# Optimization experiments

Measured on AMD Instinct MI355X. Metric: run time of the kernel, lower is better.

## Reference

```python
import jax, jax.numpy as jnp
import numpy as np
from jax import lax


def _lstm_cell(x, h, c, Wih, Whh, bih, bhh):
    # PyTorch LSTM gate order: i, f, g, o
    g = x @ Wih.T + h @ Whh.T + bih + bhh
    i, f, gg, o = jnp.split(g, 4, axis=-1)
    c_new = jax.nn.sigmoid(f) * c + jax.nn.sigmoid(i) * jnp.tanh(gg)
    h_new = jax.nn.sigmoid(o) * jnp.tanh(c_new)
    return h_new, c_new


def setup_inputs() -> dict:
    key = jax.random.key(0)
    B, Tm1, I, H, D = 2048, 32, 512, 1024, 1024
    E = H
    ks = jax.random.split(key, 20)
    s = 0.05
    return {
        'X': jax.random.normal(ks[0], (B, Tm1, I), jnp.float32),
        'y_prev': jax.random.normal(ks[1], (B, Tm1), jnp.float32),
        'enc_attn_w': jax.random.normal(ks[2], (1, 2 * H + Tm1), jnp.float32) * s,
        'enc_attn_b': jax.random.normal(ks[3], (1,), jnp.float32) * s,
        'Wih_e': jax.random.normal(ks[4], (4 * H, I), jnp.float32) * s,
        'Whh_e': jax.random.normal(ks[5], (4 * H, H), jnp.float32) * s,
        'bih_e': jax.random.normal(ks[6], (4 * H,), jnp.float32) * s,
        'bhh_e': jax.random.normal(ks[7], (4 * H,), jnp.float32) * s,
        'W1': jax.random.normal(ks[8], (E, 2 * D + E), jnp.float32) * s,
        'b1': jax.random.normal(ks[9], (E,), jnp.float32) * s,
        'W2': jax.random.normal(ks[10], (1, E), jnp.float32) * s,
        'b2': jax.random.normal(ks[11], (1,), jnp.float32) * s,
        'Wih_d': jax.random.normal(ks[12], (4 * D, 1), jnp.float32) * s,
        'Whh_d': jax.random.normal(ks[13], (4 * D, D), jnp.float32) * s,
        'bih_d': jax.random.normal(ks[14], (4 * D,), jnp.float32) * s,
        'bhh_d': jax.random.normal(ks[15], (4 * D,), jnp.float32) * s,
        'fc_w': jax.random.normal(ks[16], (1, E + 1), jnp.float32) * s,
        'fc_b': jax.random.normal(ks[17], (1,), jnp.float32) * s,
        'ff_w': jax.random.normal(ks[18], (1, D + E), jnp.float32) * s,
        'ff_b': jax.random.normal(ks[19], (1,), jnp.float32) * s,
    }


def reference(X, y_prev, enc_attn_w, enc_attn_b, Wih_e, Whh_e, bih_e, bhh_e,
              W1, b1, W2, b2, Wih_d, Whh_d, bih_d, bhh_d, fc_w, fc_b, ff_w, ff_b):
    B, Tm1, I = X.shape
    H = Whh_e.shape[1]
    D = Whh_d.shape[1]
    E = H
    dt = X.dtype

    # ---------------- Encoder ----------------
    # encoder_attn weight acts on [h; s; X_perm_row]; split for efficiency
    w_h = enc_attn_w[0, :H]
    w_s = enc_attn_w[0, H:2 * H]
    w_x = enc_attn_w[0, 2 * H:]
    # X part of attention logits is step-independent: [B, I]
    xw = jnp.einsum('bti,t->bi', X, w_x)

    def enc_step(carry, x_t):  # x_t: [B, I]
        h, s = carry
        base = h @ w_h + s @ w_s + enc_attn_b[0]          # [B]
        alpha = jax.nn.softmax(base[:, None] + xw, -1)    # softmax over input_size
        x_tilde = alpha * x_t                             # [B, I]
        h_new, s_new = _lstm_cell(x_tilde, h, s, Wih_e, Whh_e, bih_e, bhh_e)
        return (h_new, s_new), (x_tilde, h_new)

    z = jnp.zeros((B, H), dt)
    (_, _), (X_tilde, X_enc) = lax.scan(enc_step, (z, z), jnp.swapaxes(X, 0, 1))
    X_enc = jnp.swapaxes(X_enc, 0, 1)   # [B, T-1, E]

    # ---------------- Decoder ----------------
    W1_dc = W1[:, :2 * D]   # acts on [d; c]
    W1_x = W1[:, 2 * D:]    # acts on X_encoded
    Xenc_proj = jnp.einsum('bte,fe->btf', X_enc, W1_x) + b1  # [B, T-1, E]
    w2 = W2[0]

    def dec_step(carry, y_t):  # y_t: [B]
        d, c = carry
        pre = jnp.concatenate([d, c], -1) @ W1_dc.T          # [B, E]
        scores = jnp.tanh(pre[:, None, :] + Xenc_proj) @ w2 + b2[0]  # [B, T-1]
        beta = jax.nn.softmax(scores, -1)
        context = jnp.einsum('bt,bte->be', beta, X_enc)      # [B, E]
        y_tilde = context @ fc_w[0, :E] + y_t * fc_w[0, E] + fc_b[0]  # [B]
        d_new, c_new = _lstm_cell(y_tilde[:, None], d, c, Wih_d, Whh_d, bih_d, bhh_d)
        return (d_new, c_new), context

    zd = jnp.zeros((B, D), dt)
    (d, _), contexts = lax.scan(dec_step, (zd, zd), y_prev.T)
    context = contexts[-1]                                   # [B, E]
    y_pred = jnp.concatenate([d, context], -1) @ ff_w[0] + ff_b[0]  # [B]
    return y_pred[:, None]
```

## Files before the change

### kernel.cpp

```cpp
#include <hip/hip_runtime.h>
#include <cstddef>
#include <cstdint>


#define B_ 2048
#define T_ 32
#define I_ 512
#define H_ 1024
#define G_ 4096
#define E_ 1024

typedef unsigned short u16;
typedef float f32x4 __attribute__((ext_vector_type(4)));
typedef short bf16x8 __attribute__((ext_vector_type(8)));
typedef __attribute__((address_space(1))) const void gv_t;
typedef __attribute__((address_space(3))) void lv_t;

__device__ __forceinline__ float bf2f(u16 u) {
    union { float f; unsigned v; } w; w.v = ((unsigned)u) << 16; return w.f;
}
__device__ __forceinline__ u16 f2bf(float f) {
    union { float f; unsigned v; } w; w.f = f;
    unsigned r = w.v + 0x7fff + ((w.v >> 16) & 1);
    return (u16)(r >> 16);
}
template <typename T>
__device__ __forceinline__ float ld1(const T* p) {
    if constexpr (sizeof(T) == 4) return *(const float*)p;
    else return bf2f(*(const u16*)p);
}
template <typename T>
__device__ __forceinline__ float4 ld4(const T* p) {
    if constexpr (sizeof(T) == 4) {
        return *(const float4*)p;
    } else {
        const ushort4 u = *(const ushort4*)p;
        float4 r; r.x = bf2f(u.x); r.y = bf2f(u.y); r.z = bf2f(u.z); r.w = bf2f(u.w);
        return r;
    }
}
__device__ __forceinline__ float tf(float x) {
    const float e = __expf(2.0f * x);
    return 1.0f - 2.0f / (e + 1.0f);
}
__device__ __forceinline__ float sg(float x) {
    return 1.0f / (1.0f + __expf(-x));
}

__device__ __forceinline__ int lds_off(int row, int k) {
    return row * 128 + ((k * 2) ^ ((row & 7) << 4));
}

template <int ROWS>
__device__ __forceinline__ void stage_tile(char* lds, const u16* g,
                                           int row0, int ld, int k0, int tid)
{
    const int rb = tid >> 3, slot = tid & 7;
#pragma unroll
    for (int i = 0; i < ROWS / 32; ++i) {
        const int r = i * 32 + rb;
        const int ss = slot ^ (r & 7);
        const u16* src = g + (size_t)(row0 + r) * ld + k0 + ss * 8;
        char* dst = lds + i * 4096 + (tid & 192) * 16;
        __builtin_amdgcn_global_load_lds((gv_t*)src, (lv_t*)dst, 16, 0, 0);
    }
}

template <int BM, int BN, typename TC>
__global__ __launch_bounds__(256) void gemm_bf16(
    const u16* __restrict__ A1, int lda1, const u16* __restrict__ B1, int ldb1, int K1,
    const u16* __restrict__ A2, int lda2, const u16* __restrict__ B2, int ldb2, int K2,
    const float* __restrict__ bias1, const float* __restrict__ bias2,
    const float* __restrict__ u, const float* __restrict__ v,
    TC* __restrict__ C, int ldc)
{
    constexpr int FM = BM / 32, FN = BN / 32;
    __shared__ __align__(16) char lds[(BM + BN) * 128];
    char* ldsA = lds;
    char* ldsB = lds + BM * 128;
    const int tid = threadIdx.x;
    const int lane = tid & 63, wid = tid >> 6;
    const int wm = wid >> 1, wn = wid & 1;
    const int bm = blockIdx.y * BM, bn = blockIdx.x * BN;

    f32x4 acc[FM][FN] = {};

    for (int pair = 0; pair < 2; ++pair) {
        const u16* A = pair ? A2 : A1;
        const u16* Bw = pair ? B2 : B1;
        const int lda = pair ? lda2 : lda1;
        const int ldb = pair ? ldb2 : ldb1;
        const int K = pair ? K2 : K1;
        if (K == 0) continue;
        for (int k0 = 0; k0 < K; k0 += 64) {
            stage_tile<BM>(ldsA, A, bm, lda, k0, tid);
            stage_tile<BN>(ldsB, Bw, bn, ldb, k0, tid);
            __syncthreads();
#pragma unroll
            for (int kk = 0; kk < 64; kk += 32) {
                const int krd = kk + (lane >> 4) * 8;
                bf16x8 af[FM], bfr[FN];
#pragma unroll
                for (int i = 0; i < FM; ++i)
                    af[i] = *(const bf16x8*)(ldsA +
                        lds_off(wm * FM * 16 + i * 16 + (lane & 15), krd));
#pragma unroll
                for (int j = 0; j < FN; ++j)
                    bfr[j] = *(const bf16x8*)(ldsB +
                        lds_off(wn * FN * 16 + j * 16 + (lane & 15), krd));
#pragma unroll
                for (int i = 0; i < FM; ++i)
#pragma unroll
                    for (int j = 0; j < FN; ++j)
                        acc[i][j] = __builtin_amdgcn_mfma_f32_16x16x32_bf16(
                            af[i], bfr[j], acc[i][j], 0, 0, 0);
            }
            __syncthreads();
        }
    }

#pragma unroll
    for (int j = 0; j < FN; ++j) {
        const int col = bn + wn * FN * 16 + j * 16 + (lane & 15);
        const float bsum = (bias1 ? bias1[col] : 0.f) + (bias2 ? bias2[col] : 0.f);
        const float vv = v ? v[col] : 0.f;
#pragma unroll
        for (int i = 0; i < FM; ++i) {
#pragma unroll
            for (int r = 0; r < 4; ++r) {
                const int row = bm + wm * FM * 16 + i * 16 + (lane >> 4) * 4 + r;
                float val = acc[i][j][r] + bsum;
                if (u) val += u[row] * vv;
                if constexpr (sizeof(TC) == 4)
                    ((float*)C)[(size_t)row * ldc + col] = val;
                else
                    ((u16*)C)[(size_t)row * ldc + col] = f2bf(val);
            }
        }
    }
}

template <bool ENC>
__global__ __launch_bounds__(256) void gemm_lstm(
    const u16* __restrict__ A1, int lda1, const u16* __restrict__ B1, int K1,
    const u16* __restrict__ A2, int lda2, const u16* __restrict__ B2, int K2,
    const float* __restrict__ bias_p, const float* __restrict__ u,
    const float* __restrict__ v_p,
    float* __restrict__ c, float* __restrict__ h,
    u16* __restrict__ h_bf_out, u16* __restrict__ c_bf,
    u16* __restrict__ xenc, int t)
{
    __shared__ __align__(16) char lds[(256 + 64) * 128];
    char* ldsA = lds;
    char* ldsB = lds + 256 * 128;
    const int tid = threadIdx.x, lane = tid & 63, wid = tid >> 6;
    const int bm = blockIdx.y * 256, jg = blockIdx.x;

    f32x4 acc[4][4] = {};

    for (int pair = 0; pair < 2; ++pair) {
        const u16* A = pair ? A2 : A1;
        const u16* Bw = pair ? B2 : B1;
        const int lda = pair ? lda2 : lda1;
        const int K = pair ? K2 : K1;
        if (K == 0) continue;
        for (int k0 = 0; k0 < K; k0 += 64) {
            stage_tile<256>(ldsA, A, bm, lda, k0, tid);
            stage_tile<64>(ldsB, Bw, jg * 64, K, k0, tid);
            __syncthreads();
#pragma unroll
            for (int kk = 0; kk < 64; kk += 32) {
                const int krd = kk + (lane >> 4) * 8;
                bf16x8 af[4], bfr[4];
#pragma unroll
                for (int i = 0; i < 4; ++i)
                    af[i] = *(const bf16x8*)(ldsA +
                        lds_off(wid * 64 + i * 16 + (lane & 15), krd));
#pragma unroll
                for (int g = 0; g < 4; ++g)
                    bfr[g] = *(const bf16x8*)(ldsB +
                        lds_off(g * 16 + (lane & 15), krd));
#pragma unroll
                for (int i = 0; i < 4; ++i)
#pragma unroll
                    for (int g = 0; g < 4; ++g)
                        acc[i][g] = __builtin_amdgcn_mfma_f32_16x16x32_bf16(
                            af[i], bfr[g], acc[i][g], 0, 0, 0);
            }
            __syncthreads();
        }
    }

    const int jlo = lane & 15;
    const int j = jg * 16 + jlo;
    float bs[4], vv[4];
#pragma unroll
    for (int g = 0; g < 4; ++g) {
        const int col = jg * 64 + g * 16 + jlo;
        bs[g] = bias_p[col];
        vv[g] = ENC ? 0.f : v_p[col];
    }
#pragma unroll
    for (int i = 0; i < 4; ++i) {
#pragma unroll
        for (int r = 0; r < 4; ++r) {
            const int row = bm + wid * 64 + i * 16 + (lane >> 4) * 4 + r;
            float gi = acc[i][0][r] + bs[0];
            float gf = acc[i][1][r] + bs[1];
            float gg = acc[i][2][r] + bs[2];
            float go = acc[i][3][r] + bs[3];
            if constexpr (!ENC) {
                const float uy = u[row];
                gi += uy * vv[0]; gf += uy * vv[1];
                gg += uy * vv[2]; go += uy * vv[3];
            }
            const size_t idx = (size_t)row * 1024 + j;
            const float cn = sg(gf) * c[idx] + sg(gi) * tf(gg);
            const float hn = sg(go) * tf(cn);
            c[idx] = cn;
            h_bf_out[idx] = f2bf(hn);
            if constexpr (ENC) {
                xenc[(((size_t)row * T_ + t) << 10) + j] = f2bf(hn);
            } else {
                h[idx] = hn;
                c_bf[idx] = f2bf(cn);
            }
        }
    }
}

__global__ __launch_bounds__(256) void attn_prep(
    const float* __restrict__ X, const float* __restrict__ eaw, float* __restrict__ alpha)
{
    const int b = blockIdx.x, tid = threadIdx.x;
    __shared__ float wx[T_];
    __shared__ float red[4];
    if (tid < T_) wx[tid] = eaw[2 * H_ + tid];
    __syncthreads();
    const float* xb = X + (size_t)b * T_ * I_;
    float a0 = 0.0f, a1 = 0.0f;
#pragma unroll
    for (int t = 0; t < T_; ++t) {
        a0 = fmaf(xb[t * I_ + tid], wx[t], a0);
        a1 = fmaf(xb[t * I_ + tid + 256], wx[t], a1);
    }
    float m = fmaxf(a0, a1);
#pragma unroll
    for (int off = 32; off; off >>= 1) m = fmaxf(m, __shfl_down(m, off));
    if ((tid & 63) == 0) red[tid >> 6] = m;
    __syncthreads();
    m = fmaxf(fmaxf(red[0], red[1]), fmaxf(red[2], red[3]));
    __syncthreads();
    const float e0 = expf(a0 - m), e1 = expf(a1 - m);
    float ssum = e0 + e1;
#pragma unroll
    for (int off = 32; off; off >>= 1) ssum += __shfl_down(ssum, off);
    if ((tid & 63) == 0) red[tid >> 6] = ssum;
    __syncthreads();
    const float inv = 1.0f / (red[0] + red[1] + red[2] + red[3]);
    alpha[(size_t)b * I_ + tid]       = e0 * inv;
    alpha[(size_t)b * I_ + tid + 256] = e1 * inv;
}

__global__ __launch_bounds__(256) void build_xt(
    const float* __restrict__ X, const float* __restrict__ alpha, u16* __restrict__ Xt)
{
    const int il = blockIdx.x * 256 + threadIdx.x;
    const int t = blockIdx.y;
    const int b = il >> 9, i = il & 511;
    const float val = alpha[il] * X[(((size_t)b * T_ + t) << 9) + i];
    Xt[((size_t)t * B_ + b) * I_ + i] = f2bf(val);
}

__global__ __launch_bounds__(256) void split_w1(
    const float* __restrict__ W1, u16* __restrict__ W1dc, u16* __restrict__ W1x)
{
    const int id = blockIdx.x * 256 + threadIdx.x;
    const int f = id / 768, c4 = (id % 768) * 4;
    const float4 v = *(const float4*)(W1 + (size_t)f * 3072 + c4);
    ushort4 s; s.x = f2bf(v.x); s.y = f2bf(v.y); s.z = f2bf(v.z); s.w = f2bf(v.w);
    if (c4 < 2048) *(ushort4*)(W1dc + (size_t)f * 2048 + c4) = s;
    else           *(ushort4*)(W1x  + (size_t)f * 1024 + (c4 - 2048)) = s;
}

__global__ __launch_bounds__(256) void perm_w(
    const float* __restrict__ src, u16* __restrict__ dst, int K)
{
    const int id = blockIdx.x * 256 + threadIdx.x;
    const int K4 = K >> 2;
    const int np = id / K4, c4 = (id % K4) * 4;
    const int gate = (np >> 4) & 3;
    const int j = (np >> 6) * 16 + (np & 15);
    const int n = (gate << 10) + j;
    const float4 v = *(const float4*)(src + (size_t)n * K + c4);
    ushort4 s; s.x = f2bf(v.x); s.y = f2bf(v.y); s.z = f2bf(v.z); s.w = f2bf(v.w);
    *(ushort4*)(dst + (size_t)np * K + c4) = s;
}

__global__ __launch_bounds__(256) void perm_bv(
    const float* __restrict__ b1, const float* __restrict__ b2,
    const float* __restrict__ wv, float* __restrict__ bias_p, float* __restrict__ wv_p)
{
    const int np = blockIdx.x * 256 + threadIdx.x;
    const int gate = (np >> 4) & 3;
    const int j = (np >> 6) * 16 + (np & 15);
    const int n = (gate << 10) + j;
    bias_p[np] = b1[n] + b2[n];
    if (wv) wv_p[np] = wv[n];
}

__global__ __launch_bounds__(256) void dec_attn_v(
    const float* __restrict__ pre, const u16* __restrict__ Xproj,
    const u16* __restrict__ Xenc, const float* __restrict__ W2,
    const float* __restrict__ b2, const float* __restrict__ fc_w,
    const float* __restrict__ fc_b, const float* __restrict__ y_prev,
    int step, float* __restrict__ ctx, float* __restrict__ ytil)
{
    const int b = blockIdx.x, tid = threadIdx.x;
    const int lane = tid & 63, w = tid >> 6;
    const int e4 = tid * 4;
    __shared__ float redw[T_][4];
    __shared__ float red[4];

    const float4 pr  = *(const float4*)(pre + (size_t)b * 1024 + e4);
    const float4 w2r = *(const float4*)(W2 + e4);
    const u16* xp = Xproj + (size_t)b * T_ * 1024;

#pragma unroll
    for (int t = 0; t < T_; ++t) {
        const ushort4 xv = *(const ushort4*)(xp + t * 1024 + e4);
        float s = tf(pr.x + bf2f(xv.x)) * w2r.x;
        s += tf(pr.y + bf2f(xv.y)) * w2r.y;
        s += tf(pr.z + bf2f(xv.z)) * w2r.z;
        s += tf(pr.w + bf2f(xv.w)) * w2r.w;
#pragma unroll
        for (int off = 32; off; off >>= 1) s += __shfl_down(s, off);
        if (lane == 0) redw[t][w] = s;
    }
    __syncthreads();

    float sc[T_];
    float mx = -1e30f;
#pragma unroll
    for (int t = 0; t < T_; ++t) {
        sc[t] = redw[t][0] + redw[t][1] + redw[t][2] + redw[t][3] + b2[0];
        mx = fmaxf(mx, sc[t]);
    }
    float ssum = 0.0f;
#pragma unroll
    for (int t = 0; t < T_; ++t) { sc[t] = __expf(sc[t] - mx); ssum += sc[t]; }
    const float inv = 1.0f / ssum;

    const u16* xe = Xenc + (size_t)b * T_ * 1024;
    float cx0 = 0.f, cx1 = 0.f, cx2 = 0.f, cx3 = 0.f;
#pragma unroll
    for (int t = 0; t < T_; ++t) {
        const ushort4 xv = *(const ushort4*)(xe + t * 1024 + e4);
        const float bt = sc[t];
        cx0 = fmaf(bt, bf2f(xv.x), cx0);
        cx1 = fmaf(bt, bf2f(xv.y), cx1);
        cx2 = fmaf(bt, bf2f(xv.z), cx2);
        cx3 = fmaf(bt, bf2f(xv.w), cx3);
    }
    float4 cv; cv.x = cx0 * inv; cv.y = cx1 * inv; cv.z = cx2 * inv; cv.w = cx3 * inv;
    *(float4*)(ctx + (size_t)b * 1024 + e4) = cv;

    const float4 fw = *(const float4*)(fc_w + e4);
    float yt = cv.x * fw.x + cv.y * fw.y + cv.z * fw.z + cv.w * fw.w;
#pragma unroll
    for (int off = 32; off; off >>= 1) yt += __shfl_down(yt, off);
    if (lane == 0) red[w] = yt;
    __syncthreads();
    if (tid == 0)
        ytil[b] = red[0] + red[1] + red[2] + red[3]
                + y_prev[(size_t)b * T_ + step] * fc_w[1024] + fc_b[0];
}

__global__ __launch_bounds__(256) void final_out(
    const float* __restrict__ d, const float* __restrict__ ctx,
    const float* __restrict__ ffw, const float* __restrict__ ffb,
    float* __restrict__ out)
{
    const int b = blockIdx.x, tid = threadIdx.x;
    float s = 0.0f;
#pragma unroll
    for (int q = 0; q < 4; ++q) {
        const int e = tid + 256 * q;
        s += d[(size_t)b * 1024 + e] * ffw[e] + ctx[(size_t)b * 1024 + e] * ffw[1024 + e];
    }
#pragma unroll
    for (int off = 32; off; off >>= 1) s += __shfl_down(s, off);
    __shared__ float red[4];
    if ((tid & 63) == 0) red[tid >> 6] = s;
    __syncthreads();
    if (tid == 0) out[b] = red[0] + red[1] + red[2] + red[3] + ffb[0];
}

template <int BM, int BN, int BK, int TM, int TN, typename TA, typename TC>
__global__ __launch_bounds__(256) void gemm(
    int M, int N,
    const TA* __restrict__ A1, int lda1, const float* __restrict__ B1, int ldb1, int K1,
    const TA* __restrict__ A2, int lda2, const float* __restrict__ B2, int ldb2, int K2,
    const float* __restrict__ ascale, int ldsc,
    const float* __restrict__ bias1, const float* __restrict__ bias2,
    const float* __restrict__ u, const float* __restrict__ v,
    TC* __restrict__ C, int ldc)
{
    constexpr int TCOLS = BN / TN;
    constexpr int KCH = BK / 4;
    constexpr int ROWS_PER_PASS = 256 / KCH;

    __shared__ float As[BK][BM + 4];
    __shared__ float Bs[BK][BN + 4];

    const int tid = threadIdx.x;
    const int tn = tid % TCOLS;
    const int tm = tid / TCOLS;
    const int bn = blockIdx.x * BN;
    const int bm = blockIdx.y * BM;
    const int lrow = tid / KCH;
    const int lkc  = (tid % KCH) * 4;

    float acc[TM][TN];
#pragma unroll
    for (int i = 0; i < TM; ++i)
#pragma unroll
        for (int j = 0; j < TN; ++j) acc[i][j] = 0.0f;

    for (int pair = 0; pair < 2; ++pair) {
        const TA* A  = pair ? A2 : A1;
        const float* Bp = pair ? B2 : B1;
        const float* sc = pair ? nullptr : ascale;
        const int lda = pair ? lda2 : lda1;
        const int ldb = pair ? ldb2 : ldb1;
        const int K   = pair ? K2 : K1;
        if (K == 0) continue;
        for (int k0 = 0; k0 < K; k0 += BK) {
            __syncthreads();
#pragma unroll
            for (int r = 0; r < BM; r += ROWS_PER_PASS) {
                const int row = bm + r + lrow;
                float4 val = ld4(A + (size_t)row * lda + (k0 + lkc));
                if (sc) {
                    const float4 s = *(const float4*)(sc + (size_t)row * ldsc + (k0 + lkc));
                    val.x *= s.x; val.y *= s.y; val.z *= s.z; val.w *= s.w;
                }
                As[lkc + 0][r + lrow] = val.x;
                As[lkc + 1][r + lrow] = val.y;
                As[lkc + 2][r + lrow] = val.z;
                As[lkc + 3][r + lrow] = val.w;
            }
#pragma unroll
            for (int r = 0; r < BN; r += ROWS_PER_PASS) {
                const float4 val = *(const float4*)(Bp + (size_t)(bn + r + lrow) * ldb + (k0 + lkc));
                Bs[lkc + 0][r + lrow] = val.x;
                Bs[lkc + 1][r + lrow] = val.y;
                Bs[lkc + 2][r + lrow] = val.z;
                Bs[lkc + 3][r + lrow] = val.w;
            }
            __syncthreads();
#pragma unroll
            for (int k = 0; k < BK; ++k) {
                float a[TM], bv[TN];
#pragma unroll
                for (int i = 0; i < TM; ++i) a[i] = As[k][tm * TM + i];
#pragma unroll
                for (int j = 0; j < TN; ++j) bv[j] = Bs[k][tn * TN + j];
#pragma unroll
                for (int i = 0; i < TM; ++i)
#pragma unroll
                    for (int j = 0; j < TN; ++j)
                        acc[i][j] = fmaf(a[i], bv[j], acc[i][j]);
            }
        }
    }

#pragma unroll
    for (int i = 0; i < TM; ++i) {
        const int m = bm + tm * TM + i;
        const float um = u ? u[m] : 0.0f;
#pragma unroll
        for (int j = 0; j < TN; j += 4) {
            const int n = bn + tn * TN + j;
            float r[4];
#pragma unroll
            for (int q = 0; q < 4; ++q) {
                float val = acc[i][j + q];
                if (bias1) val += bias1[n + q];
                if (bias2) val += bias2[n + q];
                if (u)     val += um * v[n + q];
                r[q] = val;
            }
            if constexpr (sizeof(TC) == 4) {
                float4 f; f.x = r[0]; f.y = r[1]; f.z = r[2]; f.w = r[3];
                *(float4*)((float*)C + (size_t)m * ldc + n) = f;
            } else {
                ushort4 s;
                s.x = f2bf(r[0]); s.y = f2bf(r[1]); s.z = f2bf(r[2]); s.w = f2bf(r[3]);
                *(ushort4*)((u16*)C + (size_t)m * ldc + n) = s;
            }
        }
    }
}

template <typename TX>
__global__ __launch_bounds__(256) void lstm_pw(
    const float* __restrict__ gates, float* __restrict__ h, float* __restrict__ c,
    TX* __restrict__ xenc, int t)
{
    const size_t idx = (size_t)blockIdx.x * 256 + threadIdx.x;
    const int b = (int)(idx >> 10);
    const int j = (int)(idx & 1023);
    const float* g = gates + ((size_t)b << 12);
    const float gi = g[j], gf = g[j + 1024], gg = g[j + 2048], go = g[j + 3072];
    const float si = 1.0f / (1.0f + expf(-gi));
    const float sf = 1.0f / (1.0f + expf(-gf));
    const float so = 1.0f / (1.0f + expf(-go));
    const float cn = sf * c[idx] + si * tanhf(gg);
    const float hn = so * tanhf(cn);
    c[idx] = cn;
    h[idx] = hn;
    if (xenc) {
        if constexpr (sizeof(TX) == 4) ((float*)xenc)[(((size_t)b * T_ + t) << 10) + j] = hn;
        else ((u16*)xenc)[(((size_t)b * T_ + t) << 10) + j] = f2bf(hn);
    }
}

template <typename TX>
__global__ __launch_bounds__(256) void dec_attn(
    const float* __restrict__ pre, const TX* __restrict__ Xproj,
    const TX* __restrict__ Xenc, const float* __restrict__ W2,
    const float* __restrict__ b2, const float* __restrict__ fc_w,
    const float* __restrict__ fc_b, const float* __restrict__ y_prev,
    int step, float* __restrict__ ctx, float* __restrict__ ytil)
{
    const int b = blockIdx.x, tid = threadIdx.x;
    __shared__ float red[4];
    __shared__ float sc[T_];
    float pr[4], w2r[4];
#pragma unroll
    for (int q = 0; q < 4; ++q) {
        pr[q]  = pre[(size_t)b * 1024 + tid + 256 * q];
        w2r[q] = W2[tid + 256 * q];
    }
    const TX* xp = Xproj + (size_t)b * T_ * 1024;
    for (int t = 0; t < T_; ++t) {
        float s = 0.0f;
#pragma unroll
        for (int q = 0; q < 4; ++q)
            s += tanhf(pr[q] + ld1(xp + t * 1024 + tid + 256 * q)) * w2r[q];
#pragma unroll
        for (int off = 32; off; off >>= 1) s += __shfl_down(s, off);
        if ((tid & 63) == 0) red[tid >> 6] = s;
        __syncthreads();
        if (tid == 0) sc[t] = red[0] + red[1] + red[2] + red[3] + b2[0];
        __syncthreads();
    }
    float mx = -1e30f;
#pragma unroll
    for (int t = 0; t < T_; ++t) mx = fmaxf(mx, sc[t]);
    float beta[T_];
    float ssum = 0.0f;
#pragma unroll
    for (int t = 0; t < T_; ++t) { beta[t] = expf(sc[t] - mx); ssum += beta[t]; }
    const float inv = 1.0f / ssum;
    const TX* xe = Xenc + (size_t)b * T_ * 1024;
    float cx[4] = {0.0f, 0.0f, 0.0f, 0.0f};
    for (int t = 0; t < T_; ++t) {
        const float bt = beta[t];
#pragma unroll
        for (int q = 0; q < 4; ++q)
            cx[q] = fmaf(bt, ld1(xe + t * 1024 + tid + 256 * q), cx[q]);
    }
    float yt = 0.0f;
#pragma unroll
    for (int q = 0; q < 4; ++q) {
        const float cv = cx[q] * inv;
        ctx[(size_t)b * 1024 + tid + 256 * q] = cv;
        yt += cv * fc_w[tid + 256 * q];
    }
#pragma unroll
    for (int off = 32; off; off >>= 1) yt += __shfl_down(yt, off);
    if ((tid & 63) == 0) red[tid >> 6] = yt;
    __syncthreads();
    if (tid == 0)
        ytil[b] = red[0] + red[1] + red[2] + red[3]
                + y_prev[(size_t)b * T_ + step] * fc_w[1024] + fc_b[0];
}

static void run_mfma(void* const* d_in, float* out, char* ws, hipStream_t stream)
{
    const float* X      = (const float*)d_in[0];
    const float* y_prev = (const float*)d_in[1];
    const float* eaw    = (const float*)d_in[2];
    const float* Wih_e  = (const float*)d_in[4];
    const float* Whh_e  = (const float*)d_in[5];
    const float* bih_e  = (const float*)d_in[6];
    const float* bhh_e  = (const float*)d_in[7];
    const float* W1     = (const float*)d_in[8];
    const float* b1     = (const float*)d_in[9];
    const float* W2     = (const float*)d_in[10];
    const float* b2     = (const float*)d_in[11];
    const float* Wih_d  = (const float*)d_in[12];
    const float* Whh_d  = (const float*)d_in[13];
    const float* bih_d  = (const float*)d_in[14];
    const float* bhh_d  = (const float*)d_in[15];
    const float* fc_w   = (const float*)d_in[16];
    const float* fc_b   = (const float*)d_in[17];
    const float* ff_w   = (const float*)d_in[18];
    const float* ff_b   = (const float*)d_in[19];

    auto au = [](size_t x) { return (x + 255) & ~(size_t)255; };
    char* p = ws;
    u16* Xenc   = (u16*)p;    p += au((size_t)B_ * T_ * H_ * 2);
    u16* Xt     = (u16*)p;
    u16* Xproj  = (u16*)p;    p += au((size_t)B_ * T_ * H_ * 2);
    float* h    = (float*)p;  p += au((size_t)B_ * H_ * 4);
    float* c    = (float*)p;  p += au((size_t)B_ * H_ * 4);
    u16* hbf0   = (u16*)p;    p += au((size_t)B_ * H_ * 2);
    u16* hbf1   = (u16*)p;    p += au((size_t)B_ * H_ * 2);
    u16* c_bf   = (u16*)p;    p += au((size_t)B_ * H_ * 2);
    float* pre  = (float*)p;  p += au((size_t)B_ * E_ * 4);
    float* ctx  = (float*)p;  p += au((size_t)B_ * E_ * 4);
    u16* Wih_e_p = (u16*)p;   p += au((size_t)G_ * I_ * 2);
    u16* Whh_e_p = (u16*)p;   p += au((size_t)G_ * H_ * 2);
    u16* Whh_d_p = (u16*)p;   p += au((size_t)G_ * H_ * 2);
    u16* W1dc_bf = (u16*)p;   p += au((size_t)E_ * 2048 * 2);
    u16* W1x_bf  = (u16*)p;   p += au((size_t)E_ * 1024 * 2);
    float* bias_e_p = (float*)p; p += au((size_t)G_ * 4);
    float* bias_d_p = (float*)p; p += au((size_t)G_ * 4);
    float* wv_p     = (float*)p; p += au((size_t)G_ * 4);
    float* alpha    = (float*)p; p += au((size_t)B_ * I_ * 4);
    float* ytil     = (float*)p;

    perm_w<<<(G_ * (I_ / 4)) / 256, 256, 0, stream>>>(Wih_e, Wih_e_p, I_);
    perm_w<<<(G_ * (H_ / 4)) / 256, 256, 0, stream>>>(Whh_e, Whh_e_p, H_);
    perm_w<<<(G_ * (H_ / 4)) / 256, 256, 0, stream>>>(Whh_d, Whh_d_p, H_);
    perm_bv<<<G_ / 256, 256, 0, stream>>>(bih_e, bhh_e, nullptr, bias_e_p, nullptr);
    perm_bv<<<G_ / 256, 256, 0, stream>>>(bih_d, bhh_d, Wih_d, bias_d_p, wv_p);
    split_w1<<<(E_ * 768) / 256, 256, 0, stream>>>(W1, W1dc_bf, W1x_bf);

    hipMemsetAsync(c, 0, (size_t)B_ * H_ * 4, stream);
    hipMemsetAsync(hbf0, 0, (size_t)B_ * H_ * 2, stream);

    attn_prep<<<B_, 256, 0, stream>>>(X, eaw, alpha);
    build_xt<<<dim3(B_ * I_ / 256, T_), 256, 0, stream>>>(X, alpha, Xt);

    for (int t = 0; t < T_; ++t) {
        u16* hin  = (t & 1) ? hbf1 : hbf0;
        u16* hout = (t & 1) ? hbf0 : hbf1;
        gemm_lstm<true><<<dim3(H_ / 16, B_ / 256), 256, 0, stream>>>(
            Xt + (size_t)t * B_ * I_, I_, Wih_e_p, I_,
            hin, H_, Whh_e_p, H_,
            bias_e_p, nullptr, nullptr,
            c, nullptr, hout, nullptr, Xenc, t);
    }

    gemm_bf16<128, 128, u16><<<dim3(E_ / 128, (B_ * T_) / 128), 256, 0, stream>>>(
        Xenc, H_, W1x_bf, H_, H_,
        nullptr, 0, nullptr, 0, 0,
        b1, nullptr, nullptr, nullptr, Xproj, E_);

    hipMemsetAsync(c, 0, (size_t)B_ * H_ * 4, stream);
    hipMemsetAsync(hbf0, 0, (size_t)B_ * H_ * 2, stream);
    hipMemsetAsync(c_bf, 0, (size_t)B_ * H_ * 2, stream);

    for (int t = 0; t < T_; ++t) {
        u16* hin  = (t & 1) ? hbf1 : hbf0;
        u16* hout = (t & 1) ? hbf0 : hbf1;
        gemm_bf16<128, 64, float><<<dim3(E_ / 64, B_ / 128), 256, 0, stream>>>(
            hin, H_, W1dc_bf, 2048, H_,
            c_bf, H_, W1dc_bf + 1024, 2048, H_,
            nullptr, nullptr, nullptr, nullptr, pre, E_);
        dec_attn_v<<<B_, 256, 0, stream>>>(pre, Xproj, Xenc, W2, b2, fc_w, fc_b,
                                           y_prev, t, ctx, ytil);
        gemm_lstm<false><<<dim3(H_ / 16, B_ / 256), 256, 0, stream>>>(
            hin, H_, Whh_d_p, H_,
            (const u16*)nullptr, 0, nullptr, 0,
            bias_d_p, ytil, wv_p,
            c, h, hout, c_bf, nullptr, t);
    }

    final_out<<<B_, 256, 0, stream>>>(h, ctx, ff_w, ff_b, out);
}

static void run_fallback(void* const* d_in, float* out, char* ws, hipStream_t stream)
{
    const float* X      = (const float*)d_in[0];
    const float* y_prev = (const float*)d_in[1];
    const float* eaw    = (const float*)d_in[2];
    const float* Wih_e  = (const float*)d_in[4];
    const float* Whh_e  = (const float*)d_in[5];
    const float* bih_e  = (const float*)d_in[6];
    const float* bhh_e  = (const float*)d_in[7];
    const float* W1     = (const float*)d_in[8];
    const float* b1     = (const float*)d_in[9];
    const float* W2     = (const float*)d_in[10];
    const float* b2     = (const float*)d_in[11];
    const float* Wih_d  = (const float*)d_in[12];
    const float* Whh_d  = (const float*)d_in[13];
    const float* bih_d  = (const float*)d_in[14];
    const float* bhh_d  = (const float*)d_in[15];
    const float* fc_w   = (const float*)d_in[16];
    const float* fc_b   = (const float*)d_in[17];
    const float* ff_w   = (const float*)d_in[18];
    const float* ff_b   = (const float*)d_in[19];

    auto au = [](size_t x) { return (x + 255) & ~(size_t)255; };
    char* p = ws;
    float* alpha = (float*)p;  p += au((size_t)B_ * I_ * 4);
    u16*   Xenc  = (u16*)p;    p += au((size_t)B_ * T_ * H_ * 2);
    u16*   Xproj = (u16*)p;    p += au((size_t)B_ * T_ * H_ * 2);
    float* gates = (float*)p;  p += au((size_t)B_ * G_ * 4);
    float* h     = (float*)p;  p += au((size_t)B_ * H_ * 4);
    float* c     = (float*)p;  p += au((size_t)B_ * H_ * 4);
    float* pre   = (float*)p;  p += au((size_t)B_ * E_ * 4);
    float* ctx   = (float*)p;  p += au((size_t)B_ * E_ * 4);
    float* ytil  = (float*)p;

    hipMemsetAsync(h, 0, (size_t)B_ * H_ * 4, stream);
    hipMemsetAsync(c, 0, (size_t)B_ * H_ * 4, stream);

    attn_prep<<<B_, 256, 0, stream>>>(X, eaw, alpha);

    for (int t = 0; t < T_; ++t) {
        gemm<128, 128, 16, 8, 8, float, float><<<dim3(G_ / 128, B_ / 128), 256, 0, stream>>>(
            B_, G_,
            X + (size_t)t * I_, T_ * I_, Wih_e, I_, I_,
            h, H_, Whh_e, H_, H_,
            alpha, I_,
            bih_e, bhh_e, nullptr, nullptr, gates, G_);
        lstm_pw<u16><<<(B_ * H_) / 256, 256, 0, stream>>>(gates, h, c, Xenc, t);
    }

    gemm<128, 128, 16, 8, 8, u16, u16><<<dim3(E_ / 128, (B_ * T_) / 128), 256, 0, stream>>>(
        B_ * T_, E_,
        Xenc, H_, W1 + 2048, 3072, H_,
        (const u16*)nullptr, 0, nullptr, 0, 0,
        nullptr, 0,
        b1, nullptr, nullptr, nullptr, Xproj, E_);

    hipMemsetAsync(h, 0, (size_t)B_ * H_ * 4, stream);
    hipMemsetAsync(c, 0, (size_t)B_ * H_ * 4, stream);

    for (int t = 0; t < T_; ++t) {
        gemm<64, 64, 16, 4, 4, float, float><<<dim3(E_ / 64, B_ / 64), 256, 0, stream>>>(
            B_, E_,
            h, H_, W1, 3072, H_,
            c, H_, W1 + 1024, 3072, H_,
            nullptr, 0,
            nullptr, nullptr, nullptr, nullptr, pre, E_);
        dec_attn<u16><<<B_, 256, 0, stream>>>(pre, Xproj, Xenc, W2, b2, fc_w, fc_b,
                                              y_prev, t, ctx, ytil);
        gemm<128, 128, 16, 8, 8, float, float><<<dim3(G_ / 128, B_ / 128), 256, 0, stream>>>(
            B_, G_,
            h, H_, Whh_d, H_, H_,
            (const float*)nullptr, 0, nullptr, 0, 0,
            nullptr, 0,
            bih_d, bhh_d, ytil, Wih_d, gates, G_);
        lstm_pw<float><<<(B_ * H_) / 256, 256, 0, stream>>>(gates, h, c, nullptr, t);
    }

    final_out<<<B_, 256, 0, stream>>>(h, ctx, ff_w, ff_b, out);
}

extern "C" void kernel_launch(void* const* d_in, const int* in_sizes, int n_in,
                              void* d_out, int out_size, void* d_ws, size_t ws_size,
                              hipStream_t stream)
{
    auto au = [](size_t x) { return (x + 255) & ~(size_t)255; };
    const size_t needM =
        2 * au((size_t)B_ * T_ * H_ * 2) +
        2 * au((size_t)B_ * H_ * 4) +
        3 * au((size_t)B_ * H_ * 2) +
        2 * au((size_t)B_ * E_ * 4) +
        au((size_t)G_ * I_ * 2) + 2 * au((size_t)G_ * H_ * 2) +
        au((size_t)E_ * 2048 * 2) + au((size_t)E_ * 1024 * 2) +
        3 * au((size_t)G_ * 4) +
        au((size_t)B_ * I_ * 4) +
        au((size_t)B_ * 4) + 4096;

    if (ws_size >= needM)
        run_mfma(d_in, (float*)d_out, (char*)d_ws, stream);
    else
        run_fallback(d_in, (float*)d_out, (char*)d_ws, stream);
}
```

Before: 6.636 ms.

## Fuse encoder attention prep, skip zero-state work, widen decoder attention loads

Merges attn_prep and build_xt into one kernel that keeps X in registers and writes the bf16 Xt directly, which removes the alpha buffer round trip. At t=0 it skips the recurrent GEMM terms (K=0) and the decoder pre-projection, and drops the matching memsets. The fp32 h store now happens only on the last decoder step. dec_attn_v2 uses 8-wide bf16 loads with the block split into two halves over time, and the decoder pre GEMM tile changes to 64x64. The catch is that correctness relies on gemm_lstm handling K=0 and on pre being zeroed beforehand.

```diff
diff --git a/kernel.cpp b/kernel.cpp
--- a/kernel.cpp
+++ b/kernel.cpp
@@ -13,6 +13,7 @@
 typedef unsigned short u16;
 typedef float f32x4 __attribute__((ext_vector_type(4)));
 typedef short bf16x8 __attribute__((ext_vector_type(8)));
+typedef unsigned short us8 __attribute__((ext_vector_type(8)));
 typedef __attribute__((address_space(1))) const void gv_t;
 typedef __attribute__((address_space(3))) void lv_t;
 
@@ -222,15 +223,15 @@
             if constexpr (ENC) {
                 xenc[(((size_t)row * T_ + t) << 10) + j] = f2bf(hn);
             } else {
-                h[idx] = hn;
+                if (h) h[idx] = hn;
                 c_bf[idx] = f2bf(cn);
             }
         }
     }
 }
 
-__global__ __launch_bounds__(256) void attn_prep(
-    const float* __restrict__ X, const float* __restrict__ eaw, float* __restrict__ alpha)
+__global__ __launch_bounds__(256) void attn_prep_xt(
+    const float* __restrict__ X, const float* __restrict__ eaw, u16* __restrict__ Xt)
 {
     const int b = blockIdx.x, tid = threadIdx.x;
     __shared__ float wx[T_];
@@ -238,11 +239,14 @@
     if (tid < T_) wx[tid] = eaw[2 * H_ + tid];
     __syncthreads();
     const float* xb = X + (size_t)b * T_ * I_;
+    float xv0[T_], xv1[T_];
     float a0 = 0.0f, a1 = 0.0f;
 #pragma unroll
     for (int t = 0; t < T_; ++t) {
-        a0 = fmaf(xb[t * I_ + tid], wx[t], a0);
-        a1 = fmaf(xb[t * I_ + tid + 256], wx[t], a1);
+        xv0[t] = xb[t * I_ + tid];
+        xv1[t] = xb[t * I_ + tid + 256];
+        a0 = fmaf(xv0[t], wx[t], a0);
+        a1 = fmaf(xv1[t], wx[t], a1);
     }
     float m = fmaxf(a0, a1);
 #pragma unroll
@@ -258,18 +262,13 @@
     if ((tid & 63) == 0) red[tid >> 6] = ssum;
     __syncthreads();
     const float inv = 1.0f / (red[0] + red[1] + red[2] + red[3]);
-    alpha[(size_t)b * I_ + tid]       = e0 * inv;
-    alpha[(size_t)b * I_ + tid + 256] = e1 * inv;
-}
-
-__global__ __launch_bounds__(256) void build_xt(
-    const float* __restrict__ X, const float* __restrict__ alpha, u16* __restrict__ Xt)
-{
-    const int il = blockIdx.x * 256 + threadIdx.x;
-    const int t = blockIdx.y;
-    const int b = il >> 9, i = il & 511;
-    const float val = alpha[il] * X[(((size_t)b * T_ + t) << 9) + i];
-    Xt[((size_t)t * B_ + b) * I_ + i] = f2bf(val);
+    const float al0 = e0 * inv, al1 = e1 * inv;
+#pragma unroll
+    for (int t = 0; t < T_; ++t) {
+        u16* dst = Xt + ((size_t)t * B_ + b) * I_;
+        dst[tid]       = f2bf(al0 * xv0[t]);
+        dst[tid + 256] = f2bf(al1 * xv1[t]);
+    }
 }
 
 __global__ __launch_bounds__(256) void split_w1(
@@ -309,7 +308,7 @@
     if (wv) wv_p[np] = wv[n];
 }
 
-__global__ __launch_bounds__(256) void dec_attn_v(
+__global__ __launch_bounds__(256) void dec_attn_v2(
     const float* __restrict__ pre, const u16* __restrict__ Xproj,
     const u16* __restrict__ Xenc, const float* __restrict__ W2,
     const float* __restrict__ b2, const float* __restrict__ fc_w,
@@ -318,24 +317,30 @@
 {
     const int b = blockIdx.x, tid = threadIdx.x;
     const int lane = tid & 63, w = tid >> 6;
-    const int e4 = tid * 4;
-    __shared__ float redw[T_][4];
-    __shared__ float red[4];
-
-    const float4 pr  = *(const float4*)(pre + (size_t)b * 1024 + e4);
-    const float4 w2r = *(const float4*)(W2 + e4);
+    const int half = tid >> 7, hl = tid & 127;
+    const int e8 = hl * 8;
+    __shared__ float redw[T_][2];
+    __shared__ float ctxs[128][8];
+    __shared__ float red[2];
+
+    float pr[8], w2r[8];
+    *(float4*)(pr)      = *(const float4*)(pre + (size_t)b * 1024 + e8);
+    *(float4*)(pr + 4)  = *(const float4*)(pre + (size_t)b * 1024 + e8 + 4);
+    *(float4*)(w2r)     = *(const float4*)(W2 + e8);
+    *(float4*)(w2r + 4) = *(const float4*)(W2 + e8 + 4);
+
     const u16* xp = Xproj + (size_t)b * T_ * 1024;
-
-#pragma unroll
-    for (int t = 0; t < T_; ++t) {
-        const ushort4 xv = *(const ushort4*)(xp + t * 1024 + e4);
-        float s = tf(pr.x + bf2f(xv.x)) * w2r.x;
-        s += tf(pr.y + bf2f(xv.y)) * w2r.y;
-        s += tf(pr.z + bf2f(xv.z)) * w2r.z;
-        s += tf(pr.w + bf2f(xv.w)) * w2r.w;
+#pragma unroll
+    for (int it = 0; it < 16; ++it) {
+        const int t = 2 * it + half;
+        const us8 xv = *(const us8*)(xp + t * 1024 + e8);
+        float s = 0.0f;
+#pragma unroll
+        for (int k = 0; k < 8; ++k)
+            s += tf(pr[k] + bf2f(xv[k])) * w2r[k];
 #pragma unroll
         for (int off = 32; off; off >>= 1) s += __shfl_down(s, off);
-        if (lane == 0) redw[t][w] = s;
+        if (lane == 0) redw[t][w & 1] = s;
     }
     __syncthreads();
 
@@ -343,7 +348,7 @@
     float mx = -1e30f;
 #pragma unroll
     for (int t = 0; t < T_; ++t) {
-        sc[t] = redw[t][0] + redw[t][1] + redw[t][2] + redw[t][3] + b2[0];
+        sc[t] = redw[t][0] + redw[t][1] + b2[0];
         mx = fmaxf(mx, sc[t]);
     }
     float ssum = 0.0f;
@@ -352,27 +357,42 @@
     const float inv = 1.0f / ssum;
 
     const u16* xe = Xenc + (size_t)b * T_ * 1024;
-    float cx0 = 0.f, cx1 = 0.f, cx2 = 0.f, cx3 = 0.f;
-#pragma unroll
-    for (int t = 0; t < T_; ++t) {
-        const ushort4 xv = *(const ushort4*)(xe + t * 1024 + e4);
+    float cx[8] = {};
+#pragma unroll
+    for (int it = 0; it < 16; ++it) {
+        const int t = 2 * it + half;
+        const us8 xv = *(const us8*)(xe + t * 1024 + e8);
         const float bt = sc[t];
-        cx0 = fmaf(bt, bf2f(xv.x), cx0);
-        cx1 = fmaf(bt, bf2f(xv.y), cx1);
-        cx2 = fmaf(bt, bf2f(xv.z), cx2);
-        cx3 = fmaf(bt, bf2f(xv.w), cx3);
-    }
-    float4 cv; cv.x = cx0 * inv; cv.y = cx1 * inv; cv.z = cx2 * inv; cv.w = cx3 * inv;
-    *(float4*)(ctx + (size_t)b * 1024 + e4) = cv;
-
-    const float4 fw = *(const float4*)(fc_w + e4);
-    float yt = cv.x * fw.x + cv.y * fw.y + cv.z * fw.z + cv.w * fw.w;
+#pragma unroll
+        for (int k = 0; k < 8; ++k)
+            cx[k] = fmaf(bt, bf2f(xv[k]), cx[k]);
+    }
+    if (half == 1) {
+#pragma unroll
+        for (int k = 0; k < 8; ++k) ctxs[hl][k] = cx[k];
+    }
+    __syncthreads();
+
+    float yt = 0.0f;
+    if (half == 0) {
+        float fw[8];
+        *(float4*)(fw)     = *(const float4*)(fc_w + e8);
+        *(float4*)(fw + 4) = *(const float4*)(fc_w + e8 + 4);
+        float cv[8];
+#pragma unroll
+        for (int k = 0; k < 8; ++k) {
+            cv[k] = (cx[k] + ctxs[hl][k]) * inv;
+            yt += cv[k] * fw[k];
+        }
+        *(float4*)(ctx + (size_t)b * 1024 + e8)     = *(float4*)(cv);
+        *(float4*)(ctx + (size_t)b * 1024 + e8 + 4) = *(float4*)(cv + 4);
+    }
 #pragma unroll
     for (int off = 32; off; off >>= 1) yt += __shfl_down(yt, off);
-    if (lane == 0) red[w] = yt;
+    if (lane == 0 && w < 2) red[w] = yt;
     __syncthreads();
     if (tid == 0)
-        ytil[b] = red[0] + red[1] + red[2] + red[3]
+        ytil[b] = red[0] + red[1]
                 + y_prev[(size_t)b * T_ + step] * fc_w[1024] + fc_b[0];
 }
 
@@ -394,6 +414,39 @@
     if ((tid & 63) == 0) red[tid >> 6] = s;
     __syncthreads();
     if (tid == 0) out[b] = red[0] + red[1] + red[2] + red[3] + ffb[0];
+}
+
+__global__ __launch_bounds__(256) void attn_prep(
+    const float* __restrict__ X, const float* __restrict__ eaw, float* __restrict__ alpha)
+{
+    const int b = blockIdx.x, tid = threadIdx.x;
+    __shared__ float wx[T_];
+    __shared__ float red[4];
+    if (tid < T_) wx[tid] = eaw[2 * H_ + tid];
+    __syncthreads();
+    const float* xb = X + (size_t)b * T_ * I_;
+    float a0 = 0.0f, a1 = 0.0f;
+#pragma unroll
+    for (int t = 0; t < T_; ++t) {
+        a0 = fmaf(xb[t * I_ + tid], wx[t], a0);
+        a1 = fmaf(xb[t * I_ + tid + 256], wx[t], a1);
+    }
+    float m = fmaxf(a0, a1);
+#pragma unroll
+    for (int off = 32; off; off >>= 1) m = fmaxf(m, __shfl_down(m, off));
+    if ((tid & 63) == 0) red[tid >> 6] = m;
+    __syncthreads();
+    m = fmaxf(fmaxf(red[0], red[1]), fmaxf(red[2], red[3]));
+    __syncthreads();
+    const float e0 = expf(a0 - m), e1 = expf(a1 - m);
+    float ssum = e0 + e1;
+#pragma unroll
+    for (int off = 32; off; off >>= 1) ssum += __shfl_down(ssum, off);
+    if ((tid & 63) == 0) red[tid >> 6] = ssum;
+    __syncthreads();
+    const float inv = 1.0f / (red[0] + red[1] + red[2] + red[3]);
+    alpha[(size_t)b * I_ + tid]       = e0 * inv;
+    alpha[(size_t)b * I_ + tid + 256] = e1 * inv;
 }
 
 template <int BM, int BN, int BK, int TM, int TN, typename TA, typename TC>
@@ -630,7 +683,6 @@
     float* bias_e_p = (float*)p; p += au((size_t)G_ * 4);
     float* bias_d_p = (float*)p; p += au((size_t)G_ * 4);
     float* wv_p     = (float*)p; p += au((size_t)G_ * 4);
-    float* alpha    = (float*)p; p += au((size_t)B_ * I_ * 4);
     float* ytil     = (float*)p;
 
     perm_w<<<(G_ * (I_ / 4)) / 256, 256, 0, stream>>>(Wih_e, Wih_e_p, I_);
@@ -641,17 +693,14 @@
     split_w1<<<(E_ * 768) / 256, 256, 0, stream>>>(W1, W1dc_bf, W1x_bf);
 
     hipMemsetAsync(c, 0, (size_t)B_ * H_ * 4, stream);
-    hipMemsetAsync(hbf0, 0, (size_t)B_ * H_ * 2, stream);
-
-    attn_prep<<<B_, 256, 0, stream>>>(X, eaw, alpha);
-    build_xt<<<dim3(B_ * I_ / 256, T_), 256, 0, stream>>>(X, alpha, Xt);
+    attn_prep_xt<<<B_, 256, 0, stream>>>(X, eaw, Xt);
 
     for (int t = 0; t < T_; ++t) {
         u16* hin  = (t & 1) ? hbf1 : hbf0;
         u16* hout = (t & 1) ? hbf0 : hbf1;
         gemm_lstm<true><<<dim3(H_ / 16, B_ / 256), 256, 0, stream>>>(
             Xt + (size_t)t * B_ * I_, I_, Wih_e_p, I_,
-            hin, H_, Whh_e_p, H_,
+            hin, H_, Whh_e_p, t == 0 ? 0 : H_,
             bias_e_p, nullptr, nullptr,
             c, nullptr, hout, nullptr, Xenc, t);
     }
@@ -662,23 +711,23 @@
         b1, nullptr, nullptr, nullptr, Xproj, E_);
 
     hipMemsetAsync(c, 0, (size_t)B_ * H_ * 4, stream);
-    hipMemsetAsync(hbf0, 0, (size_t)B_ * H_ * 2, stream);
-    hipMemsetAsync(c_bf, 0, (size_t)B_ * H_ * 2, stream);
+    hipMemsetAsync(pre, 0, (size_t)B_ * E_ * 4, stream);
 
     for (int t = 0; t < T_; ++t) {
         u16* hin  = (t & 1) ? hbf1 : hbf0;
         u16* hout = (t & 1) ? hbf0 : hbf1;
-        gemm_bf16<128, 64, float><<<dim3(E_ / 64, B_ / 128), 256, 0, stream>>>(
-            hin, H_, W1dc_bf, 2048, H_,
-            c_bf, H_, W1dc_bf + 1024, 2048, H_,
-            nullptr, nullptr, nullptr, nullptr, pre, E_);
-        dec_attn_v<<<B_, 256, 0, stream>>>(pre, Xproj, Xenc, W2, b2, fc_w, fc_b,
-                                           y_prev, t, ctx, ytil);
+        if (t > 0)
+            gemm_bf16<64, 64, float><<<dim3(E_ / 64, B_ / 64), 256, 0, stream>>>(
+                hin, H_, W1dc_bf, 2048, H_,
+                c_bf, H_, W1dc_bf + 1024, 2048, H_,
+                nullptr, nullptr, nullptr, nullptr, pre, E_);
+        dec_attn_v2<<<B_, 256, 0, stream>>>(pre, Xproj, Xenc, W2, b2, fc_w, fc_b,
+                                            y_prev, t, ctx, ytil);
         gemm_lstm<false><<<dim3(H_ / 16, B_ / 256), 256, 0, stream>>>(
-            hin, H_, Whh_d_p, H_,
+            hin, H_, Whh_d_p, t == 0 ? 0 : H_,
             (const u16*)nullptr, 0, nullptr, 0,
             bias_d_p, ytil, wv_p,
-            c, h, hout, c_bf, nullptr, t);
+            c, t == T_ - 1 ? h : nullptr, hout, c_bf, nullptr, t);
     }
 
     final_out<<<B_, 256, 0, stream>>>(h, ctx, ff_w, ff_b, out);
@@ -777,7 +826,6 @@
         au((size_t)G_ * I_ * 2) + 2 * au((size_t)G_ * H_ * 2) +
         au((size_t)E_ * 2048 * 2) + au((size_t)E_ * 1024 * 2) +
         3 * au((size_t)G_ * 4) +
-        au((size_t)B_ * I_ * 4) +
         au((size_t)B_ * 4) + 4096;
 
     if (ws_size >= needM)
```

Result: faster. 6.207 ms (-6.5%).
